# Optimization experiments

Measured on AMD Instinct MI355X. Metric: run time of the kernel, lower is better.

Reference implementation:

```python
import jax, jax.numpy as jnp
import numpy as np

EPS = 1e-3  # BatchNormalization epsilon


def setup_inputs() -> dict:
    key = jax.random.key(0)
    ks = jax.random.split(key, 8)
    B, H, W, C = 16, 128, 128, 128
    f = C // 2  # filters = max(1, C // 2)
    x = jax.random.normal(ks[0], (B, H, W, C), dtype=jnp.float32)
    s_in = 1.0 / np.sqrt(C)
    s_f = 1.0 / np.sqrt(f)
    return {
        "x": x,
        "Wg": jax.random.normal(ks[1], (C, f), dtype=jnp.float32) * s_in,
        "bg": jnp.zeros((f,), jnp.float32),
        "Wt": jax.random.normal(ks[2], (C, f), dtype=jnp.float32) * s_in,
        "bt": jnp.zeros((f,), jnp.float32),
        "Wp": jax.random.normal(ks[3], (C, f), dtype=jnp.float32) * s_in,
        "bp": jnp.zeros((f,), jnp.float32),
        "Wo": jax.random.normal(ks[4], (f, f), dtype=jnp.float32) * s_f,
        "bo": jnp.zeros((f,), jnp.float32),
        "gamma": jnp.ones((f,), jnp.float32),
        "beta": jnp.zeros((f,), jnp.float32),
        "moving_mean": jnp.zeros((f,), jnp.float32),
        "moving_var": jnp.ones((f,), jnp.float32),
    }


def reference(x, Wg, bg, Wt, bt, Wp, bp, Wo, bo, gamma, beta, moving_mean, moving_var):
    B, H, W, C = x.shape
    f = Wg.shape[1]
    N = H * W
    # 1x1 conv projections (NHWC): einsum over channel dim, then flatten spatial
    g = (jnp.einsum('bhwc,cf->bhwf', x, Wg) + bg).reshape(B, N, f)     # [B,N,f]
    tx = (jnp.einsum('bhwc,cf->bhwf', x, Wt) + bt).reshape(B, N, f)    # theta
    ty = (jnp.einsum('bhwc,cf->bhwf', x, Wp) + bp).reshape(B, N, f)    # phi
    # keras Dot(axes=[1,2]) on ([B,N,f], Permute->[B,f,N]) contracts the N axes
    # -> f x f Gram matrix per batch element.
    fm = jnp.einsum('bni,bnj->bij', tx, ty)                            # [B,f,f]
    fm = jax.nn.softmax(fm, axis=-1)
    # second Dot(axes=[1,2]): contract fm axis 1 (i) with g axis 2 (i) -> [B,f,N]
    z = jnp.einsum('bij,bni->bjn', fm, g)                              # [B,f,N]
    # Reshape flat-reinterprets [B, f*N] as [B,H,W,f]
    z = z.reshape(B, H, W, f)
    # output 1x1 conv (f -> f channels)
    z = jnp.einsum('bhwf,fe->bhwe', z, Wo) + bo
    # BatchNorm, inference mode (moving statistics)
    inv = gamma * jax.lax.rsqrt(moving_var + EPS)
    z = (z - moving_mean) * inv + beta
    return z
```

## Files before the change

### kernel.cpp

```cpp
#include <hip/hip_runtime.h>
#include <stdint.h>

#define B_ 16
#define H_ 128
#define W_ 128
#define C_ 128
#define F_ 64
#define N_ (H_*W_)
#define SPLITS 32
#define RPB (N_/SPLITS)
#define CH 64
#define EPSV 1e-3f

typedef __attribute__((ext_vector_type(8))) short bf16x8;
typedef __attribute__((ext_vector_type(16))) float f32x16;

__device__ __forceinline__ unsigned short f2b(float f) {
    unsigned int x = __float_as_uint(f);
    x += 0x7fffu + ((x >> 16) & 1u);
    return (unsigned short)(x >> 16);
}
__device__ __forceinline__ float b2f(unsigned short u) {
    return __uint_as_float(((unsigned int)u) << 16);
}

__global__ __launch_bounds__(256, 2)
void kS(const float* __restrict__ x, const float* __restrict__ Wg,
        const float* __restrict__ bg, unsigned short* __restrict__ g,
        float* __restrict__ Spart, float* __restrict__ cspart)
{
    __shared__ unsigned int  xsT_hi[C_][36];
    __shared__ unsigned int  xsT_lo[C_][36];
    __shared__ unsigned short xs_hi[CH][136];
    __shared__ unsigned short WgT[F_][136];

    const int tid  = threadIdx.x;
    const int lane = tid & 63;
    const int w    = tid >> 6;
    const int b    = blockIdx.x >> 5;
    const int sp   = blockIdx.x & 31;

    for (int i = tid; i < C_*F_; i += 256) {
        int c = i >> 6, f = i & 63;
        WgT[f][c] = f2b(Wg[i]);
    }

    const float* xb = x + ((size_t)b * N_ + (size_t)sp * RPB) * C_;
    unsigned short* gb = g + ((size_t)b * N_ + (size_t)sp * RPB) * F_;

    const int rowA = lane & 31;
    const int kgrp = (lane >> 5) * 8;
    const int c1b  = (w & 1) * 64;
    const int c2b  = (w >> 1) * 64;
    const int nbG  = (w & 1) * 32;
    const int fbG  = (w >> 1) * 32;

    const float bgl = bg[fbG + rowA];

    f32x16 accS[2][2];
    #pragma unroll
    for (int ti = 0; ti < 2; ++ti)
        #pragma unroll
        for (int tj = 0; tj < 2; ++tj)
            #pragma unroll
            for (int e = 0; e < 16; ++e) accS[ti][tj][e] = 0.f;
    float csum = 0.f;

    for (int ch = 0; ch < RPB/CH; ++ch) {
        const float* xc = xb + (size_t)ch * CH * C_;
        #pragma unroll
        for (int p = 0; p < 4; ++p) {
            const int idx = tid + 256*p;
            const int np  = idx & 31;
            const int c4  = (idx >> 5) * 4;
            const float* r0 = xc + (size_t)(2*np) * C_ + c4;
            float4 a = *(const float4*)r0;
            float4 q = *(const float4*)(r0 + C_);
            unsigned short ha0 = f2b(a.x), ha1 = f2b(a.y), ha2 = f2b(a.z), ha3 = f2b(a.w);
            unsigned short hb0 = f2b(q.x), hb1 = f2b(q.y), hb2 = f2b(q.z), hb3 = f2b(q.w);
            unsigned short la0 = f2b(a.x - b2f(ha0)), la1 = f2b(a.y - b2f(ha1));
            unsigned short la2 = f2b(a.z - b2f(ha2)), la3 = f2b(a.w - b2f(ha3));
            unsigned short lb0 = f2b(q.x - b2f(hb0)), lb1 = f2b(q.y - b2f(hb1));
            unsigned short lb2 = f2b(q.z - b2f(hb2)), lb3 = f2b(q.w - b2f(hb3));
            if (p == 0) __syncthreads();
            xsT_hi[c4+0][np] = (unsigned)ha0 | ((unsigned)hb0 << 16);
            xsT_hi[c4+1][np] = (unsigned)ha1 | ((unsigned)hb1 << 16);
            xsT_hi[c4+2][np] = (unsigned)ha2 | ((unsigned)hb2 << 16);
            xsT_hi[c4+3][np] = (unsigned)ha3 | ((unsigned)hb3 << 16);
            xsT_lo[c4+0][np] = (unsigned)la0 | ((unsigned)lb0 << 16);
            xsT_lo[c4+1][np] = (unsigned)la1 | ((unsigned)lb1 << 16);
            xsT_lo[c4+2][np] = (unsigned)la2 | ((unsigned)lb2 << 16);
            xsT_lo[c4+3][np] = (unsigned)la3 | ((unsigned)lb3 << 16);
            ushort4 u0; u0.x = ha0; u0.y = ha1; u0.z = ha2; u0.w = ha3;
            ushort4 u1; u1.x = hb0; u1.y = hb1; u1.z = hb2; u1.w = hb3;
            *(ushort4*)&xs_hi[2*np  ][c4] = u0;
            *(ushort4*)&xs_hi[2*np+1][c4] = u1;
        }
        __syncthreads();

        if (tid < C_) {
            #pragma unroll 8
            for (int npp = 0; npp < 32; ++npp) {
                unsigned int h = xsT_hi[tid][npp];
                unsigned int l = xsT_lo[tid][npp];
                csum += b2f((unsigned short)(h & 0xffffu)) + b2f((unsigned short)(h >> 16))
                      + b2f((unsigned short)(l & 0xffffu)) + b2f((unsigned short)(l >> 16));
            }
        }

        #pragma unroll
        for (int ks = 0; ks < 4; ++ks) {
            const int kn = ks*16 + kgrp;
            bf16x8 Ah[2], Al[2], Bh[2], Bl[2];
            #pragma unroll
            for (int t = 0; t < 2; ++t) {
                const unsigned short* rAh = (const unsigned short*)&xsT_hi[c1b + 32*t + rowA][0];
                const unsigned short* rAl = (const unsigned short*)&xsT_lo[c1b + 32*t + rowA][0];
                Ah[t] = *(const bf16x8*)(rAh + kn);
                Al[t] = *(const bf16x8*)(rAl + kn);
                const unsigned short* rBh = (const unsigned short*)&xsT_hi[c2b + 32*t + rowA][0];
                const unsigned short* rBl = (const unsigned short*)&xsT_lo[c2b + 32*t + rowA][0];
                Bh[t] = *(const bf16x8*)(rBh + kn);
                Bl[t] = *(const bf16x8*)(rBl + kn);
            }
            #pragma unroll
            for (int ti = 0; ti < 2; ++ti)
                #pragma unroll
                for (int tj = 0; tj < 2; ++tj) {
                    accS[ti][tj] = __builtin_amdgcn_mfma_f32_32x32x16_bf16(Ah[ti], Bh[tj], accS[ti][tj], 0, 0, 0);
                    accS[ti][tj] = __builtin_amdgcn_mfma_f32_32x32x16_bf16(Ah[ti], Bl[tj], accS[ti][tj], 0, 0, 0);
                    accS[ti][tj] = __builtin_amdgcn_mfma_f32_32x32x16_bf16(Al[ti], Bh[tj], accS[ti][tj], 0, 0, 0);
                }
        }

        {
            f32x16 aG;
            #pragma unroll
            for (int e = 0; e < 16; ++e) aG[e] = 0.f;
            #pragma unroll
            for (int ks = 0; ks < 8; ++ks) {
                bf16x8 av = *(const bf16x8*)&xs_hi[nbG + rowA][ks*16 + kgrp];
                bf16x8 wv = *(const bf16x8*)&WgT [fbG + rowA][ks*16 + kgrp];
                aG = __builtin_amdgcn_mfma_f32_32x32x16_bf16(av, wv, aG, 0, 0, 0);
            }
            const int fcol = fbG + (lane & 31);
            #pragma unroll
            for (int r = 0; r < 16; ++r) {
                int nloc = (r & 3) + 8*(r >> 2) + 4*(lane >> 5);
                int n = ch*CH + nbG + nloc;
                gb[(size_t)n * F_ + fcol] = f2b(aG[r] + bgl);
            }
        }
        __syncthreads();
    }

    float* so = Spart + (size_t)(b * SPLITS + sp) * (size_t)(C_ * C_);
    #pragma unroll
    for (int ti = 0; ti < 2; ++ti)
        #pragma unroll
        for (int tj = 0; tj < 2; ++tj)
            #pragma unroll
            for (int r = 0; r < 16; ++r) {
                int c1 = c1b + 32*ti + (r & 3) + 8*(r >> 2) + 4*(lane >> 5);
                int c2 = c2b + 32*tj + (lane & 31);
                so[(size_t)c1 * C_ + c2] = accS[ti][tj][r];
            }
    if (tid < C_)
        cspart[(size_t)(b * SPLITS + sp) * C_ + tid] = csum;
}

__global__ __launch_bounds__(256, 8)
void kR(const float* __restrict__ Spart, const float* __restrict__ cspart,
        float* __restrict__ Sred, float* __restrict__ csred)
{
    const int b = blockIdx.x >> 4;
    const int r = blockIdx.x & 15;
    const int f4 = r*256 + threadIdx.x;
    const float4* base = (const float4*)(Spart + (size_t)b * SPLITS * C_ * C_);
    float sx=0.f, sy=0.f, sz=0.f, sw=0.f;
    #pragma unroll 4
    for (int sp = 0; sp < SPLITS; ++sp) {
        float4 v = base[(size_t)sp * (C_*C_/4) + f4];
        sx += v.x; sy += v.y; sz += v.z; sw += v.w;
    }
    ((float4*)(Sred + (size_t)b * C_ * C_))[f4] = make_float4(sx, sy, sz, sw);

    if (r == 0 && threadIdx.x < C_) {
        float c = 0.f;
        #pragma unroll 4
        for (int sp = 0; sp < SPLITS; ++sp)
            c += cspart[((size_t)b * SPLITS + sp) * C_ + threadIdx.x];
        csred[(size_t)b * C_ + threadIdx.x] = c;
    }
}

__global__ __launch_bounds__(256, 2)
void kT(const float* __restrict__ Sred, const float* __restrict__ csred,
        const float* __restrict__ Wp, float* __restrict__ T1buf,
        float* __restrict__ T2buf)
{
    __shared__ float Ss[32][C_];
    __shared__ float Wps[C_][F_];

    const int tid = threadIdx.x;
    const int b = blockIdx.x >> 2;
    const int q = blockIdx.x & 3;

    const float4* sg = (const float4*)(Sred + ((size_t)b * C_ + q*32) * C_);
    for (int t = tid; t < 32*C_/4; t += 256) ((float4*)Ss)[t] = sg[t];
    const float4* wg = (const float4*)Wp;
    for (int t = tid; t < C_*F_/4; t += 256) ((float4*)Wps)[t] = wg[t];
    __syncthreads();

    const int lane = tid & 63;
    const int w    = tid >> 6;

    float acc[8] = {0.f,0.f,0.f,0.f,0.f,0.f,0.f,0.f};
    #pragma unroll 2
    for (int k = 0; k < C_; k += 4) {
        float w0 = Wps[k+0][lane];
        float w1 = Wps[k+1][lane];
        float w2 = Wps[k+2][lane];
        float w3 = Wps[k+3][lane];
        #pragma unroll
        for (int cl = 0; cl < 8; ++cl) {
            float4 sv = *(const float4*)&Ss[w*8 + cl][k];
            float t = acc[cl];
            t = fmaf(sv.x, w0, t);
            t = fmaf(sv.y, w1, t);
            t = fmaf(sv.z, w2, t);
            t = fmaf(sv.w, w3, t);
            acc[cl] = t;
        }
    }
    #pragma unroll
    for (int cl = 0; cl < 8; ++cl) {
        int c = q*32 + w*8 + cl;
        T1buf[((size_t)b * C_ + c) * F_ + lane] = acc[cl];
    }

    if (q == 0 && tid < F_) {
        const float* cv = csred + (size_t)b * C_;
        float s = 0.f;
        for (int k = 0; k < C_; ++k) s = fmaf(cv[k], Wps[k][tid], s);
        T2buf[(size_t)b * F_ + tid] = s;
    }
}

__global__ __launch_bounds__(256, 2)
void kF(const float* __restrict__ T1buf, const float* __restrict__ T2buf,
        const float* __restrict__ csred, const float* __restrict__ Wt,
        const float* __restrict__ bt, const float* __restrict__ bp,
        float* __restrict__ U)
{
    __shared__ float T1s[C_][F_];
    __shared__ float Wts[C_][F_];
    __shared__ float csb[C_];
    __shared__ float T2s[F_], T3s[F_], bts[F_], bps[F_];

    const int tid = threadIdx.x;
    const int b = blockIdx.x;

    for (int t = tid; t < C_*F_/4; t += 256) {
        ((float4*)T1s)[t] = ((const float4*)(T1buf + (size_t)b * C_ * F_))[t];
        ((float4*)Wts)[t] = ((const float4*)Wt)[t];
    }
    if (tid < C_) csb[tid] = csred[(size_t)b * C_ + tid];
    if (tid < F_) {
        T2s[tid] = T2buf[(size_t)b * F_ + tid];
        bts[tid] = bt[tid];
        bps[tid] = bp[tid];
    }
    __syncthreads();

    if (tid < F_) {
        float s = 0.f;
        for (int c = 0; c < C_; ++c) s = fmaf(csb[c], Wts[c][tid], s);
        T3s[tid] = s;
    }
    __syncthreads();

    const int lane = tid & 63;
    const int w    = tid >> 6;

    float acc[16];
    #pragma unroll
    for (int r = 0; r < 16; ++r) acc[r] = 0.f;

    #pragma unroll 2
    for (int c = 0; c < C_; ++c) {
        float t1 = T1s[c][lane];
        #pragma unroll
        for (int u = 0; u < 4; ++u) {
            float4 wv = *(const float4*)&Wts[c][w*16 + u*4];
            acc[u*4+0] = fmaf(wv.x, t1, acc[u*4+0]);
            acc[u*4+1] = fmaf(wv.y, t1, acc[u*4+1]);
            acc[u*4+2] = fmaf(wv.z, t1, acc[u*4+2]);
            acc[u*4+3] = fmaf(wv.w, t1, acc[u*4+3]);
        }
    }

    const float bpj = bps[lane];
    const float t2j = T2s[lane];
    #pragma unroll
    for (int r = 0; r < 16; ++r) {
        const int i = w*16 + r;
        float v = acc[r] + T3s[i]*bpj + bts[i]*(t2j + (float)N_ * bpj);
        float m = v;
        #pragma unroll
        for (int o = 32; o; o >>= 1) m = fmaxf(m, __shfl_xor(m, o));
        float e = expf(v - m);
        float s = e;
        #pragma unroll
        for (int o = 32; o; o >>= 1) s += __shfl_xor(s, o);
        U[((size_t)b * F_ + i) * F_ + lane] = e / s;
    }
}

__global__ __launch_bounds__(256, 2)
void kC(const unsigned short* __restrict__ g, const float* __restrict__ U,
        const float* __restrict__ Wo, const float* __restrict__ bo,
        const float* __restrict__ gamma_, const float* __restrict__ beta_,
        const float* __restrict__ mmean, const float* __restrict__ mvar,
        float* __restrict__ out)
{
    __shared__ __align__(16) unsigned short UT[F_][72];
    __shared__ __align__(16) unsigned short WoT[F_][72];
    __shared__ __align__(16) unsigned short M1T[4][32][72];

    const int tid  = threadIdx.x;
    const int lane = tid & 63;
    const int wv   = tid >> 6;
    const int jt   = wv & 1;
    const int et   = wv >> 1;

    const int wgrp = blockIdx.x & 15;
    const int half = (blockIdx.x >> 4) & 1;
    const int b    = blockIdx.x >> 5;

    for (int t = tid; t < 1024; t += 256) {
        const int i  = t >> 4;
        const int j4 = (t & 15) * 4;
        float4 uv = *(const float4*)(U + ((size_t)b * F_ + i) * F_ + j4);
        UT[j4+0][i] = f2b(uv.x); UT[j4+1][i] = f2b(uv.y);
        UT[j4+2][i] = f2b(uv.z); UT[j4+3][i] = f2b(uv.w);
        float4 wo4 = *(const float4*)(Wo + (size_t)i * F_ + j4);
        WoT[j4+0][i] = f2b(wo4.x); WoT[j4+1][i] = f2b(wo4.y);
        WoT[j4+2][i] = f2b(wo4.z); WoT[j4+3][i] = f2b(wo4.w);
    }
    __syncthreads();

    const int rowA = lane & 31;
    const int hi   = lane >> 5;
    const int hi8  = hi * 8;

    bf16x8 Ufr[4], WoFr[4];
    #pragma unroll
    for (int ks = 0; ks < 4; ++ks) {
        Ufr[ks]  = *(const bf16x8*)&UT [32*jt + rowA][16*ks + hi8];
        WoFr[ks] = *(const bf16x8*)&WoT[32*et + rowA][16*ks + hi8];
    }

    const int ep = 32*et + rowA;
    const float scl = gamma_[ep] * rsqrtf(mvar[ep] + EPSV);
    const float sft = (bo[ep] - mmean[ep]) * scl + beta_[ep];

    const unsigned short* gB = g + ((size_t)b * N_ + (size_t)half * (N_/2)) * F_;
    float* outB = out + (((size_t)b * H_ + half) * W_) * F_ + ep;
    const int w0 = wgrp * 8;

    unsigned short* m1row = &M1T[wv][rowA][0];

    auto gload = [&](bf16x8 (&D)[2][4], int widx) {
        const unsigned short* gw = gB + (size_t)widx * (64*F_) + (size_t)rowA * F_ + hi8;
        #pragma unroll
        for (int ft = 0; ft < 2; ++ft)
            #pragma unroll
            for (int ks = 0; ks < 4; ++ks)
                D[ft][ks] = *(const bf16x8*)(gw + ft*(32*F_) + 16*ks);
    };

    auto body = [&](bf16x8 (&G)[2][4], int widx) {
        f32x16 m0, m1, a2r;
        #pragma unroll
        for (int e = 0; e < 16; ++e) { m0[e] = 0.f; m1[e] = 0.f; a2r[e] = 0.f; }
        #pragma unroll
        for (int ks = 0; ks < 4; ++ks) {
            m0 = __builtin_amdgcn_mfma_f32_32x32x16_bf16(G[0][ks], Ufr[ks], m0, 0, 0, 0);
            m1 = __builtin_amdgcn_mfma_f32_32x32x16_bf16(G[1][ks], Ufr[ks], m1, 0, 0, 0);
        }
        #pragma unroll
        for (int r = 0; r < 16; r += 2) {
            const int e0 = (r & 3) + 8*(r >> 2) + 4*hi;
            const unsigned pw0 = (unsigned)f2b(m0[r]) | ((unsigned)f2b(m0[r+1]) << 16);
            *(unsigned int*)(m1row + e0) = pw0;
            const unsigned pw1 = (unsigned)f2b(m1[r]) | ((unsigned)f2b(m1[r+1]) << 16);
            *(unsigned int*)(m1row + 32 + e0) = pw1;
        }
        __syncthreads();
        #pragma unroll
        for (int ksg = 0; ksg < 4; ++ksg) {
            bf16x8 af = *(const bf16x8*)(m1row + 16*ksg + hi8);
            a2r = __builtin_amdgcn_mfma_f32_32x32x16_bf16(af, WoFr[ksg], a2r, 0, 0, 0);
        }
        float* ow = outB + (size_t)widx * F_ + (size_t)(64*jt + 8*hi) * (W_*F_);
        #pragma unroll
        for (int r = 0; r < 16; ++r) {
            const int off2j = 2*(r & 3) + 16*(r >> 2);
            ow[(size_t)off2j * (W_*F_)] = a2r[r] * scl + sft;
        }
        __syncthreads();
    };

    bf16x8 GA[2][4], GBf[2][4];
    gload(GA, w0);
    #pragma unroll
    for (int wi = 0; wi < 8; ++wi) {
        if (wi & 1) {
            if (wi < 7) gload(GA, w0 + wi + 1);
            body(GBf, w0 + wi);
        } else {
            if (wi < 7) gload(GBf, w0 + wi + 1);
            body(GA, w0 + wi);
        }
    }
}

extern "C" void kernel_launch(void* const* d_in, const int* in_sizes, int n_in,
                              void* d_out, int out_size, void* d_ws, size_t ws_size,
                              hipStream_t stream)
{
    const float* x  = (const float*)d_in[0];
    const float* Wg = (const float*)d_in[1];
    const float* bg = (const float*)d_in[2];
    const float* Wt = (const float*)d_in[3];
    const float* bt = (const float*)d_in[4];
    const float* Wp = (const float*)d_in[5];
    const float* bp = (const float*)d_in[6];
    const float* Wo = (const float*)d_in[7];
    const float* bo = (const float*)d_in[8];
    const float* ga = (const float*)d_in[9];
    const float* be = (const float*)d_in[10];
    const float* mm = (const float*)d_in[11];
    const float* mv = (const float*)d_in[12];
    float* out = (float*)d_out;

    char* ws = (char*)d_ws;
    unsigned short* g = (unsigned short*)ws;
    size_t off = (size_t)B_ * N_ * F_ * sizeof(unsigned short);
    float* Spart = (float*)(ws + off);
    float* T1buf = (float*)(ws + off);
    off += (size_t)B_ * SPLITS * C_ * C_ * sizeof(float);
    float* cspart = (float*)(ws + off);
    off += (size_t)B_ * SPLITS * C_ * sizeof(float);
    float* U = (float*)(ws + off);
    off += (size_t)B_ * F_ * F_ * sizeof(float);
    float* Sred = (float*)(ws + off);
    off += (size_t)B_ * C_ * C_ * sizeof(float);
    float* csred = (float*)(ws + off);
    off += (size_t)B_ * C_ * sizeof(float);
    float* T2buf = (float*)(ws + off);

    kS<<<B_ * SPLITS, 256, 0, stream>>>(x, Wg, bg, g, Spart, cspart);
    kR<<<B_ * 16, 256, 0, stream>>>(Spart, cspart, Sred, csred);
    kT<<<B_ * 4, 256, 0, stream>>>(Sred, csred, Wp, T1buf, T2buf);
    kF<<<B_, 256, 0, stream>>>(T1buf, T2buf, csred, Wt, bt, bp, U);
    kC<<<B_ * 2 * (W_/8), 256, 0, stream>>>(g, U, Wo, bo, ga, be, mm, mv, out);
}
```

Measured before the change: 110.5 us.

## Prefetch next x chunk into registers and hold Wg fragments in registers in kS

The kS kernel now loads the next 64-row chunk of x into registers while MFMA work on the current chunk proceeds. This is register double-buffering meant to hide global load latency. The Wg tile is staged through shared memory once, then kept as per-lane bf16 fragments in registers, and its shared buffer is reused for the x hi tile. The smaller shared-memory footprint lets occupancy rise to 3 blocks per CU. The trade is higher register pressure from the prefetch buffers and the weight fragments under a tighter launch bound, which risks spills.

```diff
diff --git a/kernel.cpp b/kernel.cpp
--- a/kernel.cpp
+++ b/kernel.cpp
@@ -24,15 +24,14 @@
     return __uint_as_float(((unsigned int)u) << 16);
 }
 
-__global__ __launch_bounds__(256, 2)
+__global__ __launch_bounds__(256, 3)
 void kS(const float* __restrict__ x, const float* __restrict__ Wg,
         const float* __restrict__ bg, unsigned short* __restrict__ g,
         float* __restrict__ Spart, float* __restrict__ cspart)
 {
     __shared__ unsigned int  xsT_hi[C_][36];
     __shared__ unsigned int  xsT_lo[C_][36];
-    __shared__ unsigned short xs_hi[CH][136];
-    __shared__ unsigned short WgT[F_][136];
+    __shared__ __align__(16) unsigned short xs_pool[CH][136];
 
     const int tid  = threadIdx.x;
     const int lane = tid & 63;
@@ -40,13 +39,11 @@
     const int b    = blockIdx.x >> 5;
     const int sp   = blockIdx.x & 31;
 
-    for (int i = tid; i < C_*F_; i += 256) {
-        int c = i >> 6, f = i & 63;
-        WgT[f][c] = f2b(Wg[i]);
-    }
-
     const float* xb = x + ((size_t)b * N_ + (size_t)sp * RPB) * C_;
     unsigned short* gb = g + ((size_t)b * N_ + (size_t)sp * RPB) * F_;
+
+    const int np  = tid & 31;
+    const int c4b = (tid >> 5) * 4;
 
     const int rowA = lane & 31;
     const int kgrp = (lane >> 5) * 8;
@@ -57,6 +54,25 @@
 
     const float bgl = bg[fbG + rowA];
 
+    float4 ra[4], rq[4];
+    #pragma unroll
+    for (int p = 0; p < 4; ++p) {
+        const float* r0 = xb + (size_t)(2*np) * C_ + c4b + 32*p;
+        ra[p] = *(const float4*)r0;
+        rq[p] = *(const float4*)(r0 + C_);
+    }
+
+    for (int i = tid; i < C_*F_; i += 256) {
+        int c = i >> 6, f = i & 63;
+        xs_pool[f][c] = f2b(Wg[i]);
+    }
+    __syncthreads();
+    bf16x8 wgfr[8];
+    #pragma unroll
+    for (int ks = 0; ks < 8; ++ks)
+        wgfr[ks] = *(const bf16x8*)&xs_pool[fbG + rowA][ks*16 + kgrp];
+    __syncthreads();
+
     f32x16 accS[2][2];
     #pragma unroll
     for (int ti = 0; ti < 2; ++ti)
@@ -67,22 +83,18 @@
     float csum = 0.f;
 
     for (int ch = 0; ch < RPB/CH; ++ch) {
-        const float* xc = xb + (size_t)ch * CH * C_;
+        if (ch) __syncthreads();
+
         #pragma unroll
         for (int p = 0; p < 4; ++p) {
-            const int idx = tid + 256*p;
-            const int np  = idx & 31;
-            const int c4  = (idx >> 5) * 4;
-            const float* r0 = xc + (size_t)(2*np) * C_ + c4;
-            float4 a = *(const float4*)r0;
-            float4 q = *(const float4*)(r0 + C_);
+            const int c4 = c4b + 32*p;
+            float4 a = ra[p], q = rq[p];
             unsigned short ha0 = f2b(a.x), ha1 = f2b(a.y), ha2 = f2b(a.z), ha3 = f2b(a.w);
             unsigned short hb0 = f2b(q.x), hb1 = f2b(q.y), hb2 = f2b(q.z), hb3 = f2b(q.w);
             unsigned short la0 = f2b(a.x - b2f(ha0)), la1 = f2b(a.y - b2f(ha1));
             unsigned short la2 = f2b(a.z - b2f(ha2)), la3 = f2b(a.w - b2f(ha3));
             unsigned short lb0 = f2b(q.x - b2f(hb0)), lb1 = f2b(q.y - b2f(hb1));
             unsigned short lb2 = f2b(q.z - b2f(hb2)), lb3 = f2b(q.w - b2f(hb3));
-            if (p == 0) __syncthreads();
             xsT_hi[c4+0][np] = (unsigned)ha0 | ((unsigned)hb0 << 16);
             xsT_hi[c4+1][np] = (unsigned)ha1 | ((unsigned)hb1 << 16);
             xsT_hi[c4+2][np] = (unsigned)ha2 | ((unsigned)hb2 << 16);
@@ -93,10 +105,20 @@
             xsT_lo[c4+3][np] = (unsigned)la3 | ((unsigned)lb3 << 16);
             ushort4 u0; u0.x = ha0; u0.y = ha1; u0.z = ha2; u0.w = ha3;
             ushort4 u1; u1.x = hb0; u1.y = hb1; u1.z = hb2; u1.w = hb3;
-            *(ushort4*)&xs_hi[2*np  ][c4] = u0;
-            *(ushort4*)&xs_hi[2*np+1][c4] = u1;
+            *(ushort4*)&xs_pool[2*np  ][c4] = u0;
+            *(ushort4*)&xs_pool[2*np+1][c4] = u1;
         }
         __syncthreads();
+
+        if (ch < RPB/CH - 1) {
+            const float* xc = xb + (size_t)(ch+1) * CH * C_;
+            #pragma unroll
+            for (int p = 0; p < 4; ++p) {
+                const float* r0 = xc + (size_t)(2*np) * C_ + c4b + 32*p;
+                ra[p] = *(const float4*)r0;
+                rq[p] = *(const float4*)(r0 + C_);
+            }
+        }
 
         if (tid < C_) {
             #pragma unroll 8
@@ -105,6 +127,24 @@
                 unsigned int l = xsT_lo[tid][npp];
                 csum += b2f((unsigned short)(h & 0xffffu)) + b2f((unsigned short)(h >> 16))
                       + b2f((unsigned short)(l & 0xffffu)) + b2f((unsigned short)(l >> 16));
+            }
+        }
+
+        {
+            f32x16 aG;
+            #pragma unroll
+            for (int e = 0; e < 16; ++e) aG[e] = 0.f;
+            #pragma unroll
+            for (int ks = 0; ks < 8; ++ks) {
+                bf16x8 av = *(const bf16x8*)&xs_pool[nbG + rowA][ks*16 + kgrp];
+                aG = __builtin_amdgcn_mfma_f32_32x32x16_bf16(av, wgfr[ks], aG, 0, 0, 0);
+            }
+            const int fcol = fbG + (lane & 31);
+            #pragma unroll
+            for (int r = 0; r < 16; ++r) {
+                int nloc = (r & 3) + 8*(r >> 2) + 4*(lane >> 5);
+                int n = ch*CH + nbG + nloc;
+                gb[(size_t)n * F_ + fcol] = f2b(aG[r] + bgl);
             }
         }
 
@@ -132,26 +172,6 @@
                     accS[ti][tj] = __builtin_amdgcn_mfma_f32_32x32x16_bf16(Al[ti], Bh[tj], accS[ti][tj], 0, 0, 0);
                 }
         }
-
-        {
-            f32x16 aG;
-            #pragma unroll
-            for (int e = 0; e < 16; ++e) aG[e] = 0.f;
-            #pragma unroll
-            for (int ks = 0; ks < 8; ++ks) {
-                bf16x8 av = *(const bf16x8*)&xs_hi[nbG + rowA][ks*16 + kgrp];
-                bf16x8 wv = *(const bf16x8*)&WgT [fbG + rowA][ks*16 + kgrp];
-                aG = __builtin_amdgcn_mfma_f32_32x32x16_bf16(av, wv, aG, 0, 0, 0);
-            }
-            const int fcol = fbG + (lane & 31);
-            #pragma unroll
-            for (int r = 0; r < 16; ++r) {
-                int nloc = (r & 3) + 8*(r >> 2) + 4*(lane >> 5);
-                int n = ch*CH + nbG + nloc;
-                gb[(size_t)n * F_ + fcol] = f2b(aG[r] + bgl);
-            }
-        }
-        __syncthreads();
     }
 
     float* so = Spart + (size_t)(b * SPLITS + sp) * (size_t)(C_ * C_);
```

Result: slower. 139.2 us (+26.0%).

## Stage g projection through LDS for coalesced stores and keep Wg fragments in registers

Applied to the files above, without the earlier changes.

The kS kernel now loads its Wg bf16 fragments into registers once, instead of re-reading a dedicated WgT LDS array every chunk. The g projection is written to a new LDS tile gT and flushed to global memory one chunk later as 16-byte vector stores, replacing scattered 2-byte stores. The g MFMA is moved ahead of the Gram MFMAs, and the end-of-loop barrier is removed by reusing the existing barriers. The aim is less uncoalesced global write traffic and less LDS pressure, at the cost of extra VGPRs for the weight fragments and an LDS round-trip for g.

```diff
diff --git a/kernel.cpp b/kernel.cpp
--- a/kernel.cpp
+++ b/kernel.cpp
@@ -31,8 +31,8 @@
 {
     __shared__ unsigned int  xsT_hi[C_][36];
     __shared__ unsigned int  xsT_lo[C_][36];
-    __shared__ unsigned short xs_hi[CH][136];
-    __shared__ unsigned short WgT[F_][136];
+    __shared__ __align__(16) unsigned short xs_pool[CH][136];
+    __shared__ __align__(16) unsigned short gT[CH][72];
 
     const int tid  = threadIdx.x;
     const int lane = tid & 63;
@@ -40,16 +40,12 @@
     const int b    = blockIdx.x >> 5;
     const int sp   = blockIdx.x & 31;
 
-    for (int i = tid; i < C_*F_; i += 256) {
-        int c = i >> 6, f = i & 63;
-        WgT[f][c] = f2b(Wg[i]);
-    }
-
     const float* xb = x + ((size_t)b * N_ + (size_t)sp * RPB) * C_;
     unsigned short* gb = g + ((size_t)b * N_ + (size_t)sp * RPB) * F_;
 
     const int rowA = lane & 31;
-    const int kgrp = (lane >> 5) * 8;
+    const int hiL  = lane >> 5;
+    const int kgrp = hiL * 8;
     const int c1b  = (w & 1) * 64;
     const int c2b  = (w >> 1) * 64;
     const int nbG  = (w & 1) * 32;
@@ -57,6 +53,17 @@
 
     const float bgl = bg[fbG + rowA];
 
+    for (int i = tid; i < C_*F_; i += 256) {
+        int c = i >> 6, f = i & 63;
+        xs_pool[f][c] = f2b(Wg[i]);
+    }
+    __syncthreads();
+    bf16x8 wgfr[8];
+    #pragma unroll
+    for (int ks = 0; ks < 8; ++ks)
+        wgfr[ks] = *(const bf16x8*)&xs_pool[fbG + rowA][ks*16 + kgrp];
+    __syncthreads();
+
     f32x16 accS[2][2];
     #pragma unroll
     for (int ti = 0; ti < 2; ++ti)
@@ -65,6 +72,9 @@
             #pragma unroll
             for (int e = 0; e < 16; ++e) accS[ti][tj][e] = 0.f;
     float csum = 0.f;
+
+    const int sr = tid >> 2;
+    const int sc = (tid & 3) * 16;
 
     for (int ch = 0; ch < RPB/CH; ++ch) {
         const float* xc = xb + (size_t)ch * CH * C_;
@@ -93,8 +103,16 @@
             xsT_lo[c4+3][np] = (unsigned)la3 | ((unsigned)lb3 << 16);
             ushort4 u0; u0.x = ha0; u0.y = ha1; u0.z = ha2; u0.w = ha3;
             ushort4 u1; u1.x = hb0; u1.y = hb1; u1.z = hb2; u1.w = hb3;
-            *(ushort4*)&xs_hi[2*np  ][c4] = u0;
-            *(ushort4*)&xs_hi[2*np+1][c4] = u1;
+            *(ushort4*)&xs_pool[2*np  ][c4] = u0;
+            *(ushort4*)&xs_pool[2*np+1][c4] = u1;
+        }
+
+        if (ch) {
+            uint4 v0 = *(const uint4*)&gT[sr][sc];
+            uint4 v1 = *(const uint4*)&gT[sr][sc + 8];
+            unsigned short* dst = gb + (size_t)((ch-1)*CH + sr) * F_ + sc;
+            *(uint4*)dst       = v0;
+            *(uint4*)(dst + 8) = v1;
         }
         __syncthreads();
 
@@ -105,6 +123,23 @@
                 unsigned int l = xsT_lo[tid][npp];
                 csum += b2f((unsigned short)(h & 0xffffu)) + b2f((unsigned short)(h >> 16))
                       + b2f((unsigned short)(l & 0xffffu)) + b2f((unsigned short)(l >> 16));
+            }
+        }
+
+        {
+            f32x16 aG;
+            #pragma unroll
+            for (int e = 0; e < 16; ++e) aG[e] = 0.f;
+            #pragma unroll
+            for (int ks = 0; ks < 8; ++ks) {
+                bf16x8 av = *(const bf16x8*)&xs_pool[nbG + rowA][ks*16 + kgrp];
+                aG = __builtin_amdgcn_mfma_f32_32x32x16_bf16(av, wgfr[ks], aG, 0, 0, 0);
+            }
+            const int fcol = fbG + rowA;
+            #pragma unroll
+            for (int r = 0; r < 16; ++r) {
+                int nloc = (r & 3) + 8*(r >> 2) + 4*hiL;
+                gT[nbG + nloc][fcol] = f2b(aG[r] + bgl);
             }
         }
 
@@ -132,37 +167,26 @@
                     accS[ti][tj] = __builtin_amdgcn_mfma_f32_32x32x16_bf16(Al[ti], Bh[tj], accS[ti][tj], 0, 0, 0);
                 }
         }
-
-        {
-            f32x16 aG;
-            #pragma unroll
-            for (int e = 0; e < 16; ++e) aG[e] = 0.f;
-            #pragma unroll
-            for (int ks = 0; ks < 8; ++ks) {
-                bf16x8 av = *(const bf16x8*)&xs_hi[nbG + rowA][ks*16 + kgrp];
-                bf16x8 wv = *(const bf16x8*)&WgT [fbG + rowA][ks*16 + kgrp];
-                aG = __builtin_amdgcn_mfma_f32_32x32x16_bf16(av, wv, aG, 0, 0, 0);
-            }
-            const int fcol = fbG + (lane & 31);
+    }
+
+    __syncthreads();
+    {
+        uint4 v0 = *(const uint4*)&gT[sr][sc];
+        uint4 v1 = *(const uint4*)&gT[sr][sc + 8];
+        unsigned short* dst = gb + (size_t)((RPB/CH - 1)*CH + sr) * F_ + sc;
+        *(uint4*)dst       = v0;
+        *(uint4*)(dst + 8) = v1;
+    }
+
+    float* so = Spart + (size_t)(b * SPLITS + sp) * (size_t)(C_ * C_);
+    #pragma unroll
+    for (int ti = 0; ti < 2; ++ti)
+        #pragma unroll
+        for (int tj = 0; tj < 2; ++tj)
             #pragma unroll
             for (int r = 0; r < 16; ++r) {
-                int nloc = (r & 3) + 8*(r >> 2) + 4*(lane >> 5);
-                int n = ch*CH + nbG + nloc;
-                gb[(size_t)n * F_ + fcol] = f2b(aG[r] + bgl);
-            }
-        }
-        __syncthreads();
-    }
-
-    float* so = Spart + (size_t)(b * SPLITS + sp) * (size_t)(C_ * C_);
-    #pragma unroll
-    for (int ti = 0; ti < 2; ++ti)
-        #pragma unroll
-        for (int tj = 0; tj < 2; ++tj)
-            #pragma unroll
-            for (int r = 0; r < 16; ++r) {
-                int c1 = c1b + 32*ti + (r & 3) + 8*(r >> 2) + 4*(lane >> 5);
-                int c2 = c2b + 32*tj + (lane & 31);
+                int c1 = c1b + 32*ti + (r & 3) + 8*(r >> 2) + 4*hiL;
+                int c2 = c2b + 32*tj + rowA;
                 so[(size_t)c1 * C_ + c2] = accS[ti][tj][r];
             }
     if (tid < C_)
```

New measurement: 110.2 us. No clear change (-0.3%).
